# Kernel optimization log

Hardware: AMD Instinct MI355X
Metric: run time of the kernel (lower is better)

Reference implementation:

```python
import jax, jax.numpy as jnp
import numpy as np

B, P, NP, D, DS, M, K = 2, 4000, 4096, 64, 64, 512, 8
NX, NY = 432, 496
HW = NY * NX


def _per_batch(points, pillars, pillars_scale, idx, W):
    # points: [NP, D], pillars: [P, D], pillars_scale: [P, DS], idx: [P] in [0, HW)
    # --- get_score: top-k point attention per pillar ---
    score = jax.nn.softmax(points @ pillars.T, axis=0)                # [NP, P], softmax over points
    top_idx = jax.lax.top_k(jax.lax.stop_gradient(score).T, K)[1]     # [P, K]
    pts_pos = points[top_idx]                                         # [P, K, D]
    agg = jax.nn.softmax(jnp.einsum('pd,pkd->pk', pillars, pts_pos), axis=1)
    pos_point = jnp.einsum('pk,pkd->pd', jax.lax.stop_gradient(agg), pts_pos)  # [P, D]
    # --- memory unit: top-k memory-item attention per pillar ---
    att = jax.nn.softmax(pillars @ W.T, axis=1)                       # [P, M]
    midx = jax.lax.top_k(jax.lax.stop_gradient(att), K)[1]            # [P, K]
    mem_pos = W[midx]                                                 # [P, K, D]
    magg = jax.nn.softmax(jnp.einsum('pd,pkd->pk', pillars, mem_pos), axis=1)
    pos_mem = jnp.einsum('pk,pkd->pd', magg, mem_pos)                 # [P, D]
    # --- scatter into dense BEV grids ---
    sp_point = jnp.zeros((2 * D, HW), pillars.dtype).at[:, idx].set(
        jnp.concatenate([pillars, pos_point], axis=1).T)
    sp = jnp.zeros((2 * D, HW), pillars.dtype).at[:, idx].set(
        jnp.concatenate([jax.lax.stop_gradient(pillars), pos_mem], axis=1).T)
    sp_scale = jnp.zeros((DS, HW), pillars_scale.dtype).at[:, idx].set(pillars_scale.T)
    return sp, sp_point, sp_scale, pos_point, pos_mem


def setup_inputs() -> dict:
    key = jax.random.key(0)
    k1, k2, k3, k4, k5 = jax.random.split(key, 5)
    return {
        'pillar_features': jax.random.normal(k1, (B, P, D), jnp.float32),
        'pillar_scale_features': jax.random.normal(k2, (B, P, DS), jnp.float32),
        'point_features': jax.random.normal(k3, (B, NP, D), jnp.float32),
        'memory_weight': jax.random.normal(k4, (M, D), jnp.float32),
        'indices': jax.random.randint(k5, (B, P), 0, HW, jnp.int32),
    }


def reference(pillar_features, pillar_scale_features, point_features, memory_weight, indices):
    sp, sp_point, sp_scale, pos_point, pos_mem = jax.vmap(
        _per_batch, in_axes=(0, 0, 0, 0, None))(
        point_features, pillar_features, pillar_scale_features, indices, memory_weight)
    spatial_features = sp.reshape(B, 2 * D, NY, NX)
    spatial_features_point = sp_point.reshape(B, 2 * D, NY, NX)
    spatial_scale_features = sp_scale.reshape(B, DS, NY, NX)
    point_positive_features = pos_point.reshape(B * P, D)
    memory_positive_features = pos_mem.reshape(B * P, D)
    return (spatial_features, spatial_features_point, spatial_scale_features,
            point_positive_features, memory_positive_features)
```

## Files before the change

kernel.cpp:

```cpp
#include <hip/hip_runtime.h>

#define B_     2
#define P_TOT  4000
#define NP_TOT 4096
#define D_     64
#define M_     512
#define HW_TOT 214272
#define J4     53568

#define O0 0UL
#define O1 54853632UL
#define O2 109707264UL
#define O3 137134080UL
#define O4 137646080UL

typedef __attribute__((ext_vector_type(8))) short bb8;
typedef __attribute__((ext_vector_type(4))) float f32x4;

__device__ __forceinline__ void fma4(float4& a, const float4& x, const float4& y) {
  a.x = fmaf(x.x, y.x, a.x);
  a.y = fmaf(x.y, y.y, a.y);
  a.z = fmaf(x.z, y.z, a.z);
  a.w = fmaf(x.w, y.w, a.w);
}

__device__ __forceinline__ void insert8(float sc, int n, float s[8], int ix[8]) {
  float cs = sc; int ci = n;
#pragma unroll
  for (int i = 0; i < 8; ++i) {
    bool gt = cs > s[i];
    float ts = s[i]; int ti = ix[i];
    s[i]  = gt ? cs : ts;  ix[i] = gt ? ci : ti;
    cs    = gt ? ts : cs;  ci    = gt ? ti : ci;
  }
}

__device__ __forceinline__ void split_bf16(float x, short& h, short& l) {
  unsigned fb = __float_as_uint(x);
  unsigned hb = fb & 0xFFFF0000u;
  float lof = x - __uint_as_float(hb);
  h = (short)(hb >> 16);
  l = (short)(__float_as_uint(lof) >> 16);
}

__global__ __launch_bounds__(256) void cvt_planes(
    const float* __restrict__ src, short* __restrict__ hi, short* __restrict__ lo, int n4)
{
  int t = blockIdx.x * 256 + threadIdx.x;
  if (t >= n4) return;
  float4 v = ((const float4*)src)[t];
  float x[4] = {v.x, v.y, v.z, v.w};
  short h[4], l[4];
#pragma unroll
  for (int j = 0; j < 4; ++j) split_bf16(x[j], h[j], l[j]);
  ((short4*)hi)[t] = make_short4(h[0], h[1], h[2], h[3]);
  ((short4*)lo)[t] = make_short4(l[0], l[1], l[2], l[3]);
}

__global__ __launch_bounds__(256) void topk_mfma(
    const float* __restrict__ pillars,
    const short* __restrict__ phi, const short* __restrict__ plo,
    float* __restrict__ ws_sc, int* __restrict__ ws_ix)
{
  const int tid = threadIdx.x;
  const int pt = blockIdx.x, ch = blockIdx.y, b = blockIdx.z;
  const int lane = tid & 63, wv = tid >> 6;
  const int sub = lane & 15, quad = lane >> 4;

  int prow = pt * 64 + wv * 16 + sub;
  if (prow >= P_TOT) prow = P_TOT - 1;
  const float* ap = pillars + ((size_t)(b * P_TOT) + prow) * D_;
  bb8 Ah0, Ah1, Al0, Al1;
  {
    const float4* a4 = (const float4*)(ap + quad * 8);
    const float4* b4 = (const float4*)(ap + 32 + quad * 8);
    float4 t0 = a4[0], t1 = a4[1], t2 = b4[0], t3 = b4[1];
    float av[16] = {t0.x, t0.y, t0.z, t0.w, t1.x, t1.y, t1.z, t1.w,
                    t2.x, t2.y, t2.z, t2.w, t3.x, t3.y, t3.z, t3.w};
#pragma unroll
    for (int j = 0; j < 8; ++j) {
      short h, l;
      split_bf16(av[j], h, l);     Ah0[j] = h; Al0[j] = l;
      split_bf16(av[8 + j], h, l); Ah1[j] = h; Al1[j] = l;
    }
  }

  float sv[4][8]; int iv[4][8];
#pragma unroll
  for (int r = 0; r < 4; ++r)
#pragma unroll
    for (int k = 0; k < 8; ++k) { sv[r][k] = -1e30f; iv[r][k] = 0; }

  const size_t bofs = ((size_t)(b * NP_TOT) + ch * 512) * D_;
  const short* bh = phi + bofs;
  const short* bl = plo + bofs;

#pragma unroll 2
  for (int it = 0; it < 32; ++it) {
    const int nr = it * 16 + sub;
    const short* rh = bh + nr * D_;
    const short* rl = bl + nr * D_;
    bb8 Bh0 = *(const bb8*)(rh + quad * 8);
    bb8 Bh1 = *(const bb8*)(rh + 32 + quad * 8);
    bb8 Bl0 = *(const bb8*)(rl + quad * 8);
    bb8 Bl1 = *(const bb8*)(rl + 32 + quad * 8);
    f32x4 acc = {0.f, 0.f, 0.f, 0.f};
    acc = __builtin_amdgcn_mfma_f32_16x16x32_bf16(Al0, Bh0, acc, 0, 0, 0);
    acc = __builtin_amdgcn_mfma_f32_16x16x32_bf16(Al1, Bh1, acc, 0, 0, 0);
    acc = __builtin_amdgcn_mfma_f32_16x16x32_bf16(Ah0, Bl0, acc, 0, 0, 0);
    acc = __builtin_amdgcn_mfma_f32_16x16x32_bf16(Ah1, Bl1, acc, 0, 0, 0);
    acc = __builtin_amdgcn_mfma_f32_16x16x32_bf16(Ah0, Bh0, acc, 0, 0, 0);
    acc = __builtin_amdgcn_mfma_f32_16x16x32_bf16(Ah1, Bh1, acc, 0, 0, 0);
    const int ng = ch * 512 + nr;
#pragma unroll
    for (int r = 0; r < 4; ++r) {
      float sc = acc[r];
      if (sc > sv[r][7]) insert8(sc, ng, sv[r], iv[r]);
    }
  }

  const int pbase = pt * 64 + wv * 16 + quad * 4;
#pragma unroll
  for (int r = 0; r < 4; ++r) {
    const int pg = pbase + r;
    float out_s = 0.f; int out_i = 0;
#pragma unroll
    for (int k = 0; k < 8; ++k) {
      unsigned fb = __float_as_uint(sv[r][0]);
      unsigned mk = (fb & 0x80000000u) ? ~fb : (fb | 0x80000000u);
      unsigned key = (mk & 0xFFFFFFF0u) | (unsigned)sub;
#pragma unroll
      for (int off = 1; off < 16; off <<= 1) {
        unsigned ok = (unsigned)__shfl_xor((int)key, off);
        key = key > ok ? key : ok;
      }
      const int wsub = (int)(key & 15u);
      const int wlane = (lane & 48) | wsub;
      float wsc = __shfl(sv[r][0], wlane);
      int   wix = __shfl(iv[r][0], wlane);
      if (sub == wsub) {
#pragma unroll
        for (int i2 = 0; i2 < 7; ++i2) { sv[r][i2] = sv[r][i2 + 1]; iv[r][i2] = iv[r][i2 + 1]; }
        sv[r][7] = -1e30f;
      }
      if (sub == k) { out_s = wsc; out_i = wix; }
    }
    if (sub < 8 && pg < P_TOT) {
      const size_t base = ((size_t)(b * P_TOT) + pg) * 64 + ch * 8 + sub;
      ws_sc[base] = out_s; ws_ix[base] = out_i;
    }
  }
}

__global__ __launch_bounds__(256) void topk_chunk(
    const float* __restrict__ pillars, const float* __restrict__ src,
    float* __restrict__ ws_sc, int* __restrict__ ws_ix,
    int src_batch_stride, int n_tiles)
{
  __shared__ float lds_pts[64 * 64];
  __shared__ float cs_lds[32 * 65];
  __shared__ int   ci_lds[32 * 65];

  const int tid = threadIdx.x;
  const int pt = blockIdx.x, ch = blockIdx.y, b = blockIdx.z;
  const int pp = tid & 31, sg = tid >> 5;
  const int p = pt * 32 + pp;

  const float4* prow = (const float4*)(pillars + ((size_t)(b * P_TOT + p)) * D_);
  float4 pl[16];
#pragma unroll
  for (int i = 0; i < 16; ++i) pl[i] = prow[i];

  float s[8]; int ix[8];
#pragma unroll
  for (int i = 0; i < 8; ++i) { s[i] = -1e30f; ix[i] = 0; }

  const int n_base = ch * (n_tiles * 64);
  const float* srcb = src + (size_t)b * src_batch_stride;
  const int r0 = tid >> 2, seg = tid & 3;

  for (int t = 0; t < n_tiles; ++t) {
    const float4* g = (const float4*)(srcb + ((size_t)(n_base + t * 64 + r0)) * D_ + seg * 16);
    float4* dst4 = (float4*)(lds_pts + r0 * 64 + seg * 16);
    dst4[0] = g[0]; dst4[1] = g[1]; dst4[2] = g[2]; dst4[3] = g[3];
    __syncthreads();

#pragma unroll
    for (int r = 0; r < 8; ++r) {
      const int row = sg * 8 + r;
      const float4* q = (const float4*)(lds_pts + row * 64);
      float4 a0 = {0,0,0,0}, a1 = {0,0,0,0}, a2 = {0,0,0,0}, a3 = {0,0,0,0};
#pragma unroll
      for (int i = 0; i < 4; ++i) {
        fma4(a0, pl[i*4+0], q[i*4+0]);
        fma4(a1, pl[i*4+1], q[i*4+1]);
        fma4(a2, pl[i*4+2], q[i*4+2]);
        fma4(a3, pl[i*4+3], q[i*4+3]);
      }
      float sc = ((a0.x + a1.x) + (a2.x + a3.x)) + ((a0.y + a1.y) + (a2.y + a3.y))
               + ((a0.z + a1.z) + (a2.z + a3.z)) + ((a0.w + a1.w) + (a2.w + a3.w));
      int n = n_base + t * 64 + row;
      if (sc > s[7]) insert8(sc, n, s, ix);
    }
    __syncthreads();
  }

#pragma unroll
  for (int k = 0; k < 8; ++k) {
    cs_lds[pp * 65 + sg * 8 + k] = s[k];
    ci_lds[pp * 65 + sg * 8 + k] = ix[k];
  }
  __syncthreads();
  if (tid < 32) {
    float ms[8]; int mi[8];
#pragma unroll
    for (int i = 0; i < 8; ++i) { ms[i] = -1e30f; mi[i] = 0; }
    for (int k = 0; k < 64; ++k) {
      float sc = cs_lds[tid * 65 + k];
      int   ii = ci_lds[tid * 65 + k];
      if (sc > ms[7]) insert8(sc, ii, ms, mi);
    }
    const int p2 = pt * 32 + tid;
    size_t base = ((size_t)(b * P_TOT + p2)) * 64 + ch * 8;
#pragma unroll
    for (int k = 0; k < 8; ++k) { ws_sc[base + k] = ms[k]; ws_ix[base + k] = mi[k]; }
  }
}

__global__ __launch_bounds__(256) void finalize_topk(
    const float* __restrict__ src, int src_batch_stride,
    const float* __restrict__ ws_sc, const int* __restrict__ ws_ix,
    float* __restrict__ outp)
{
  const int tid = threadIdx.x;
  const int lane = tid & 63, wv = tid >> 6;
  const int gp = blockIdx.x * 4 + wv;
  const int b = (gp >= P_TOT) ? 1 : 0;
  const size_t cb = (size_t)gp * 64;

  float ss = ws_sc[cb + lane];
  const int myix = ws_ix[cb + lane];

  float wsc[8]; int wix[8];
#pragma unroll
  for (int k = 0; k < 8; ++k) {
    float cv = ss; int cl = lane;
#pragma unroll
    for (int off = 32; off >= 1; off >>= 1) {
      float ov = __shfl_xor(cv, off);
      int   ol = __shfl_xor(cl, off);
      if (ov > cv || (ov == cv && ol < cl)) { cv = ov; cl = ol; }
    }
    wsc[k] = cv;
    wix[k] = __shfl(myix, cl);
    if (lane == cl) ss = -1e30f;
  }

  const float m = wsc[0];
  float e[8], Z = 0.f;
#pragma unroll
  for (int k = 0; k < 8; ++k) { e[k] = expf(wsc[k] - m); Z += e[k]; }
  const float inv = 1.0f / Z;

  const float* sb = src + (size_t)b * src_batch_stride;
  float acc = 0.f;
#pragma unroll
  for (int k = 0; k < 8; ++k)
    acc = fmaf(e[k] * inv, sb[(size_t)wix[k] * 64 + lane], acc);
  outp[cb + lane] = acc;
}

__global__ __launch_bounds__(256) void build_owner(
    const int* __restrict__ indices, int* __restrict__ owner)
{
  int t = blockIdx.x * 256 + threadIdx.x;
  if (t >= B_ * P_TOT) return;
  int b = (t >= P_TOT) ? 1 : 0;
  int p = t - b * P_TOT;
  atomicMax(&owner[b * HW_TOT + indices[t]], p);
}

__global__ __launch_bounds__(256) void scatter_out(
    const float* __restrict__ pillars, const float* __restrict__ scale,
    const float* __restrict__ pos_point, const float* __restrict__ pos_mem,
    const int* __restrict__ owner, float* __restrict__ out)
{
  const int j4 = blockIdx.x * 256 + threadIdx.x;
  if (j4 >= J4) return;
  const int c = blockIdx.y, b = blockIdx.z;

  const int4 own = ((const int4*)owner)[(size_t)b * J4 + j4];

  const float* srcb;
  size_t d4;
  int cc;
  if (c < 128) {
    cc = (c < 64) ? c : (c - 64);
    srcb = ((c < 64) ? pillars : pos_mem) + (size_t)b * (P_TOT * D_);
    d4 = (size_t)(b * 128 + c) * J4 + j4;
  } else if (c < 256) {
    const int c1 = c - 128;
    cc = (c1 < 64) ? c1 : (c1 - 64);
    srcb = ((c1 < 64) ? pillars : pos_point) + (size_t)b * (P_TOT * D_);
    d4 = (O1 / 4) + (size_t)(b * 128 + c1) * J4 + j4;
  } else {
    cc = c - 256;
    srcb = scale + (size_t)b * (P_TOT * D_);
    d4 = (O2 / 4) + (size_t)(b * 64 + cc) * J4 + j4;
  }

  float4 v = make_float4(0.f, 0.f, 0.f, 0.f);
  if ((own.x & own.y & own.z & own.w) >= 0) {
    if (own.x >= 0) v.x = srcb[(size_t)own.x * 64 + cc];
    if (own.y >= 0) v.y = srcb[(size_t)own.y * 64 + cc];
    if (own.z >= 0) v.z = srcb[(size_t)own.z * 64 + cc];
    if (own.w >= 0) v.w = srcb[(size_t)own.w * 64 + cc];
  }
  ((float4*)out)[d4] = v;
}

extern "C" void kernel_launch(void* const* d_in, const int* in_sizes, int n_in,
                              void* d_out, int out_size, void* d_ws, size_t ws_size,
                              hipStream_t stream) {
  const float* pillars = (const float*)d_in[0];
  const float* scale   = (const float*)d_in[1];
  const float* points  = (const float*)d_in[2];
  const float* W       = (const float*)d_in[3];
  const int*   indices = (const int*)d_in[4];
  float* out = (float*)d_out;

  float* ws_pts_sc = (float*)d_ws;
  int*   ws_pts_ix = (int*)d_ws + 512000;
  float* ws_mem_sc = (float*)d_ws + 1024000;
  int*   ws_mem_ix = (int*)d_ws + 1536000;
  int*   owner     = (int*)d_ws + 2048000;
  short* phi       = (short*)((int*)d_ws + 2480000);
  short* plo       = (short*)((int*)d_ws + 2760000);

  hipMemsetAsync(owner, 0xFF, (size_t)B_ * HW_TOT * sizeof(int), stream);
  build_owner<<<32, 256, 0, stream>>>(indices, owner);

  cvt_planes<<<512, 256, 0, stream>>>(points, phi, plo, (B_ * NP_TOT * D_) / 4);

  topk_mfma<<<dim3(63, 8, 2), 256, 0, stream>>>(pillars, phi, plo, ws_pts_sc, ws_pts_ix);

  topk_chunk<<<dim3(125, 8, 2), 256, 0, stream>>>(
      pillars, W, ws_mem_sc, ws_mem_ix, 0, 1);

  finalize_topk<<<2000, 256, 0, stream>>>(points, NP_TOT * D_, ws_pts_sc, ws_pts_ix, out + O3);
  finalize_topk<<<2000, 256, 0, stream>>>(W, 0, ws_mem_sc, ws_mem_ix, out + O4);

  scatter_out<<<dim3(210, 320, 2), 256, 0, stream>>>(
      pillars, scale, out + O3, out + O4, owner, out);
}
```

Baseline: 698.2 us.

## Scatter all channels per thread with vectorized row gathers

Restructures the dense-grid scatter so each thread handles a group of 64 channels for four pixels instead of one channel. It loads source rows as float4 and transposes them into channel-major float4 stores. This removes the repeated owner-index reads and the scalar strided gathers across 320 channel blocks. The trade-offs are fewer threads in flight, more registers per thread, and unconditional loads of row 0 for empty pixels.

```diff
diff --git a/kernel.cpp b/kernel.cpp
--- a/kernel.cpp
+++ b/kernel.cpp
@@ -287,36 +287,38 @@
 {
   const int j4 = blockIdx.x * 256 + threadIdx.x;
   if (j4 >= J4) return;
-  const int c = blockIdx.y, b = blockIdx.z;
+  const int ph = blockIdx.y, b = blockIdx.z;
 
   const int4 own = ((const int4*)owner)[(size_t)b * J4 + j4];
 
-  const float* srcb;
-  size_t d4;
-  int cc;
-  if (c < 128) {
-    cc = (c < 64) ? c : (c - 64);
-    srcb = ((c < 64) ? pillars : pos_mem) + (size_t)b * (P_TOT * D_);
-    d4 = (size_t)(b * 128 + c) * J4 + j4;
-  } else if (c < 256) {
-    const int c1 = c - 128;
-    cc = (c1 < 64) ? c1 : (c1 - 64);
-    srcb = ((c1 < 64) ? pillars : pos_point) + (size_t)b * (P_TOT * D_);
-    d4 = (O1 / 4) + (size_t)(b * 128 + c1) * J4 + j4;
-  } else {
-    cc = c - 256;
-    srcb = scale + (size_t)b * (P_TOT * D_);
-    d4 = (O2 / 4) + (size_t)(b * 64 + cc) * J4 + j4;
-  }
-
-  float4 v = make_float4(0.f, 0.f, 0.f, 0.f);
-  if ((own.x & own.y & own.z & own.w) >= 0) {
-    if (own.x >= 0) v.x = srcb[(size_t)own.x * 64 + cc];
-    if (own.y >= 0) v.y = srcb[(size_t)own.y * 64 + cc];
-    if (own.z >= 0) v.z = srcb[(size_t)own.z * 64 + cc];
-    if (own.w >= 0) v.w = srcb[(size_t)own.w * 64 + cc];
-  }
-  ((float4*)out)[d4] = v;
+  const float* src;
+  size_t ob4;
+  const size_t bo = (size_t)b * (P_TOT * D_);
+  if (ph == 0)      { src = pillars   + bo; ob4 = (size_t)(b * 128)      * J4; }
+  else if (ph == 1) { src = pos_mem   + bo; ob4 = (size_t)(b * 128 + 64) * J4; }
+  else if (ph == 2) { src = pillars   + bo; ob4 = 13713408UL + (size_t)(b * 128)      * J4; }
+  else if (ph == 3) { src = pos_point + bo; ob4 = 13713408UL + (size_t)(b * 128 + 64) * J4; }
+  else              { src = scale     + bo; ob4 = 27426816UL + (size_t)(b * 64)       * J4; }
+
+  const float4* s4 = (const float4*)src;
+  const size_t rx = (size_t)(own.x < 0 ? 0 : own.x) * 16;
+  const size_t ry = (size_t)(own.y < 0 ? 0 : own.y) * 16;
+  const size_t rz = (size_t)(own.z < 0 ? 0 : own.z) * 16;
+  const size_t rw = (size_t)(own.w < 0 ? 0 : own.w) * 16;
+  const float4 z4 = make_float4(0.f, 0.f, 0.f, 0.f);
+  float4* o4 = (float4*)out + ob4 + j4;
+
+#pragma unroll 4
+  for (int cg = 0; cg < 16; ++cg) {
+    float4 vx = s4[rx + cg]; if (own.x < 0) vx = z4;
+    float4 vy = s4[ry + cg]; if (own.y < 0) vy = z4;
+    float4 vz = s4[rz + cg]; if (own.z < 0) vz = z4;
+    float4 vw = s4[rw + cg]; if (own.w < 0) vw = z4;
+    o4[(size_t)(4 * cg + 0) * J4] = make_float4(vx.x, vy.x, vz.x, vw.x);
+    o4[(size_t)(4 * cg + 1) * J4] = make_float4(vx.y, vy.y, vz.y, vw.y);
+    o4[(size_t)(4 * cg + 2) * J4] = make_float4(vx.z, vy.z, vz.z, vw.z);
+    o4[(size_t)(4 * cg + 3) * J4] = make_float4(vx.w, vy.w, vz.w, vw.w);
+  }
 }
 
 extern "C" void kernel_launch(void* const* d_in, const int* in_sizes, int n_in,
@@ -350,6 +352,6 @@
   finalize_topk<<<2000, 256, 0, stream>>>(points, NP_TOT * D_, ws_pts_sc, ws_pts_ix, out + O3);
   finalize_topk<<<2000, 256, 0, stream>>>(W, 0, ws_mem_sc, ws_mem_ix, out + O4);
 
-  scatter_out<<<dim3(210, 320, 2), 256, 0, stream>>>(
+  scatter_out<<<dim3(210, 5, 2), 256, 0, stream>>>(
       pillars, scale, out + O3, out + O4, owner, out);
 }
```

After: 710.8 us. No clear change (+1.8%).

## Fuse scatter channels into one pass and merge small prep/finalize launches

Applied to the files above, without the earlier changes.

Scatter now handles all five output planes for one channel per thread, reading the owner map once instead of five times and reusing the pillar gather for both spatial outputs, with nontemporal stores for the large dense output. The cvt_planes and build_owner kernels are merged into one prep launch, and the two finalize launches become one 2D grid. This is meant to cut owner-map reads, redundant gathers and launch overhead, in exchange for more registers per scatter thread and fewer blocks in that grid.

```diff
diff --git a/kernel.cpp b/kernel.cpp
--- a/kernel.cpp
+++ b/kernel.cpp
@@ -43,18 +43,26 @@
   l = (short)(__float_as_uint(lof) >> 16);
 }
 
-__global__ __launch_bounds__(256) void cvt_planes(
-    const float* __restrict__ src, short* __restrict__ hi, short* __restrict__ lo, int n4)
-{
-  int t = blockIdx.x * 256 + threadIdx.x;
-  if (t >= n4) return;
-  float4 v = ((const float4*)src)[t];
-  float x[4] = {v.x, v.y, v.z, v.w};
-  short h[4], l[4];
-#pragma unroll
-  for (int j = 0; j < 4; ++j) split_bf16(x[j], h[j], l[j]);
-  ((short4*)hi)[t] = make_short4(h[0], h[1], h[2], h[3]);
-  ((short4*)lo)[t] = make_short4(l[0], l[1], l[2], l[3]);
+__global__ __launch_bounds__(256) void prep(
+    const float* __restrict__ points, short* __restrict__ hi, short* __restrict__ lo,
+    const int* __restrict__ indices, int* __restrict__ owner)
+{
+  if (blockIdx.x < 512) {
+    int t = blockIdx.x * 256 + threadIdx.x;
+    float4 v = ((const float4*)points)[t];
+    float x[4] = {v.x, v.y, v.z, v.w};
+    short h[4], l[4];
+#pragma unroll
+    for (int j = 0; j < 4; ++j) split_bf16(x[j], h[j], l[j]);
+    ((short4*)hi)[t] = make_short4(h[0], h[1], h[2], h[3]);
+    ((short4*)lo)[t] = make_short4(l[0], l[1], l[2], l[3]);
+  } else {
+    int t = (blockIdx.x - 512) * 256 + threadIdx.x;
+    if (t >= B_ * P_TOT) return;
+    int b = (t >= P_TOT) ? 1 : 0;
+    int p = t - b * P_TOT;
+    atomicMax(&owner[b * HW_TOT + indices[t]], p);
+  }
 }
 
 __global__ __launch_bounds__(256) void topk_mfma(
@@ -227,16 +235,23 @@
   }
 }
 
-__global__ __launch_bounds__(256) void finalize_topk(
-    const float* __restrict__ src, int src_batch_stride,
-    const float* __restrict__ ws_sc, const int* __restrict__ ws_ix,
-    float* __restrict__ outp)
+__global__ __launch_bounds__(256) void finalize2(
+    const float* __restrict__ points, const float* __restrict__ W,
+    const float* __restrict__ ws_sc_p, const int* __restrict__ ws_ix_p,
+    const float* __restrict__ ws_sc_m, const int* __restrict__ ws_ix_m,
+    float* __restrict__ out_p, float* __restrict__ out_m)
 {
   const int tid = threadIdx.x;
   const int lane = tid & 63, wv = tid >> 6;
   const int gp = blockIdx.x * 4 + wv;
   const int b = (gp >= P_TOT) ? 1 : 0;
   const size_t cb = (size_t)gp * 64;
+  const bool mem = (blockIdx.y == 1);
+
+  const float* ws_sc = mem ? ws_sc_m : ws_sc_p;
+  const int*   ws_ix = mem ? ws_ix_m : ws_ix_p;
+  const float* sb    = mem ? W : (points + (size_t)b * (NP_TOT * D_));
+  float*       outp  = mem ? out_m : out_p;
 
   float ss = ws_sc[cb + lane];
   const int myix = ws_ix[cb + lane];
@@ -262,7 +277,6 @@
   for (int k = 0; k < 8; ++k) { e[k] = expf(wsc[k] - m); Z += e[k]; }
   const float inv = 1.0f / Z;
 
-  const float* sb = src + (size_t)b * src_batch_stride;
   float acc = 0.f;
 #pragma unroll
   for (int k = 0; k < 8; ++k)
@@ -270,17 +284,7 @@
   outp[cb + lane] = acc;
 }
 
-__global__ __launch_bounds__(256) void build_owner(
-    const int* __restrict__ indices, int* __restrict__ owner)
-{
-  int t = blockIdx.x * 256 + threadIdx.x;
-  if (t >= B_ * P_TOT) return;
-  int b = (t >= P_TOT) ? 1 : 0;
-  int p = t - b * P_TOT;
-  atomicMax(&owner[b * HW_TOT + indices[t]], p);
-}
-
-__global__ __launch_bounds__(256) void scatter_out(
+__global__ __launch_bounds__(256) void scatter5(
     const float* __restrict__ pillars, const float* __restrict__ scale,
     const float* __restrict__ pos_point, const float* __restrict__ pos_mem,
     const int* __restrict__ owner, float* __restrict__ out)
@@ -291,32 +295,36 @@
 
   const int4 own = ((const int4*)owner)[(size_t)b * J4 + j4];
 
-  const float* srcb;
-  size_t d4;
-  int cc;
-  if (c < 128) {
-    cc = (c < 64) ? c : (c - 64);
-    srcb = ((c < 64) ? pillars : pos_mem) + (size_t)b * (P_TOT * D_);
-    d4 = (size_t)(b * 128 + c) * J4 + j4;
-  } else if (c < 256) {
-    const int c1 = c - 128;
-    cc = (c1 < 64) ? c1 : (c1 - 64);
-    srcb = ((c1 < 64) ? pillars : pos_point) + (size_t)b * (P_TOT * D_);
-    d4 = (O1 / 4) + (size_t)(b * 128 + c1) * J4 + j4;
-  } else {
-    cc = c - 256;
-    srcb = scale + (size_t)b * (P_TOT * D_);
-    d4 = (O2 / 4) + (size_t)(b * 64 + cc) * J4 + j4;
-  }
-
-  float4 v = make_float4(0.f, 0.f, 0.f, 0.f);
+  const size_t bo = (size_t)b * (P_TOT * D_);
+  const float* sp = pillars   + bo;
+  const float* sm = pos_mem   + bo;
+  const float* sq = pos_point + bo;
+  const float* ss = scale     + bo;
+
+  f32x4 vp = {0.f, 0.f, 0.f, 0.f};
+  f32x4 vm = vp, vq = vp, vs = vp;
+
   if ((own.x & own.y & own.z & own.w) >= 0) {
-    if (own.x >= 0) v.x = srcb[(size_t)own.x * 64 + cc];
-    if (own.y >= 0) v.y = srcb[(size_t)own.y * 64 + cc];
-    if (own.z >= 0) v.z = srcb[(size_t)own.z * 64 + cc];
-    if (own.w >= 0) v.w = srcb[(size_t)own.w * 64 + cc];
-  }
-  ((float4*)out)[d4] = v;
+    const size_t rx = (size_t)(own.x < 0 ? 0 : own.x) * 64 + c;
+    const size_t ry = (size_t)(own.y < 0 ? 0 : own.y) * 64 + c;
+    const size_t rz = (size_t)(own.z < 0 ? 0 : own.z) * 64 + c;
+    const size_t rw = (size_t)(own.w < 0 ? 0 : own.w) * 64 + c;
+    vp = (f32x4){own.x < 0 ? 0.f : sp[rx], own.y < 0 ? 0.f : sp[ry],
+                 own.z < 0 ? 0.f : sp[rz], own.w < 0 ? 0.f : sp[rw]};
+    vm = (f32x4){own.x < 0 ? 0.f : sm[rx], own.y < 0 ? 0.f : sm[ry],
+                 own.z < 0 ? 0.f : sm[rz], own.w < 0 ? 0.f : sm[rw]};
+    vq = (f32x4){own.x < 0 ? 0.f : sq[rx], own.y < 0 ? 0.f : sq[ry],
+                 own.z < 0 ? 0.f : sq[rz], own.w < 0 ? 0.f : sq[rw]};
+    vs = (f32x4){own.x < 0 ? 0.f : ss[rx], own.y < 0 ? 0.f : ss[ry],
+                 own.z < 0 ? 0.f : ss[rz], own.w < 0 ? 0.f : ss[rw]};
+  }
+
+  f32x4* o4 = (f32x4*)out;
+  __builtin_nontemporal_store(vp, o4 + (size_t)(b * 128 + c)       * J4 + j4);
+  __builtin_nontemporal_store(vm, o4 + (size_t)(b * 128 + 64 + c)  * J4 + j4);
+  __builtin_nontemporal_store(vp, o4 + 13713408UL + (size_t)(b * 128 + c)      * J4 + j4);
+  __builtin_nontemporal_store(vq, o4 + 13713408UL + (size_t)(b * 128 + 64 + c) * J4 + j4);
+  __builtin_nontemporal_store(vs, o4 + 27426816UL + (size_t)(b * 64 + c)       * J4 + j4);
 }
 
 extern "C" void kernel_launch(void* const* d_in, const int* in_sizes, int n_in,
@@ -337,19 +345,18 @@
   short* phi       = (short*)((int*)d_ws + 2480000);
   short* plo       = (short*)((int*)d_ws + 2760000);
 
-  hipMemsetAsync(owner, 0xFF, (size_t)B_ * HW_TOT * sizeof(int), stream);
-  build_owner<<<32, 256, 0, stream>>>(indices, owner);
-
-  cvt_planes<<<512, 256, 0, stream>>>(points, phi, plo, (B_ * NP_TOT * D_) / 4);
+  (void)hipMemsetAsync(owner, 0xFF, (size_t)B_ * HW_TOT * sizeof(int), stream);
+
+  prep<<<544, 256, 0, stream>>>(points, phi, plo, indices, owner);
 
   topk_mfma<<<dim3(63, 8, 2), 256, 0, stream>>>(pillars, phi, plo, ws_pts_sc, ws_pts_ix);
 
   topk_chunk<<<dim3(125, 8, 2), 256, 0, stream>>>(
       pillars, W, ws_mem_sc, ws_mem_ix, 0, 1);
 
-  finalize_topk<<<2000, 256, 0, stream>>>(points, NP_TOT * D_, ws_pts_sc, ws_pts_ix, out + O3);
-  finalize_topk<<<2000, 256, 0, stream>>>(W, 0, ws_mem_sc, ws_mem_ix, out + O4);
-
-  scatter_out<<<dim3(210, 320, 2), 256, 0, stream>>>(
+  finalize2<<<dim3(2000, 2), 256, 0, stream>>>(
+      points, W, ws_pts_sc, ws_pts_ix, ws_mem_sc, ws_mem_ix, out + O3, out + O4);
+
+  scatter5<<<dim3(210, 64, 2), 256, 0, stream>>>(
       pillars, scale, out + O3, out + O4, owner, out);
 }
```

Measured after the change: 687.4 us, median of 2. About the same (-1.5%).
